# Kernel optimization log

Hardware: AMD Instinct MI355X
Metric: run time of the kernel (lower is better)

Reference implementation:

```python
import jax, jax.numpy as jnp
import numpy as np

TEMPERATURE = 0.1


def setup_inputs() -> dict:
    key = jax.random.key(0)
    k1, k2 = jax.random.split(key)
    B, D = 4096, 256
    z_i = jax.random.normal(k1, (B, D), dtype=jnp.float32)
    z_j = jax.random.normal(k2, (B, D), dtype=jnp.float32)
    return {"z_i": z_i, "z_j": z_j}


def reference(z_i, z_j):
    B = z_i.shape[0]
    N = 2 * B
    z = jnp.concatenate([z_i, z_j], axis=0)  # [N, D]
    # cosine similarity via normalize + GEMM (same math as broadcasted F.cosine_similarity)
    eps = 1e-8
    zn = z / jnp.maximum(jnp.linalg.norm(z, axis=1, keepdims=True), eps)
    sim = (zn @ zn.T) / TEMPERATURE  # [N, N]
    # positives: sim[i, (i+B) % N]
    rows = jnp.arange(N)
    pos = sim[rows, (rows + B) % N]  # [N]
    # denominator: sum of exp over all entries except the diagonal (positives included,
    # matching the original which only masks the eye)
    neg_inf = jnp.array(-jnp.inf, sim.dtype)
    sim_masked = jnp.where(jnp.eye(N, dtype=bool), neg_inf, sim)
    lse = jax.nn.logsumexp(sim_masked, axis=1)  # [N]
    loss = -(pos - lse)
    return loss.mean()
```

## Files before the change

### kernel.cpp

```cpp
#include <hip/hip_runtime.h>
#include <hip/hip_bf16.h>

typedef __bf16 bf16x8 __attribute__((ext_vector_type(8)));
typedef float  f32x4  __attribute__((ext_vector_type(4)));

#define N_TOT  8192
#define B_HALF 4096
#define D      256
#define SQK1   3.79828254f
#define LN2    0.6931471805599453f

#define RB      128
#define WROWS   32
#define CB      32
#define SLICE   512
#define NSLICE  16
#define NSTAGE  16

__global__ __launch_bounds__(256) void normalize_kernel(
    const float* __restrict__ zi, const float* __restrict__ zj,
    ushort* __restrict__ zn, float* __restrict__ out)
{
    if (blockIdx.x == 0 && threadIdx.x == 0) *out = 0.0f;
    int row  = (blockIdx.x * 256 + threadIdx.x) >> 6;
    int lane = threadIdx.x & 63;
    const float* src = (row < B_HALF) ? (zi + (size_t)row * D)
                                      : (zj + (size_t)(row - B_HALF) * D);
    float4 v = ((const float4*)src)[lane];
    float ss = v.x * v.x + v.y * v.y + v.z * v.z + v.w * v.w;
    #pragma unroll
    for (int m = 1; m < 64; m <<= 1) ss += __shfl_xor(ss, m);
    float r = SQK1 / fmaxf(sqrtf(ss), 1e-8f);
    union { ushort4 u4; __hip_bfloat16 h[4]; } o;
    o.h[0] = __float2bfloat16(v.x * r);
    o.h[1] = __float2bfloat16(v.y * r);
    o.h[2] = __float2bfloat16(v.z * r);
    o.h[3] = __float2bfloat16(v.w * r);
    ((ushort4*)zn)[(size_t)row * (D / 4) + lane] = o.u4;
}

__global__ __launch_bounds__(256) void fused_kernel(
    const ushort* __restrict__ zn,
    float* __restrict__ spartial,
    float* __restrict__ posdot)
{
    __shared__ ushort lds[2][CB * 256];

    int tid  = threadIdx.x;
    int lane = tid & 63;
    int w    = tid >> 6;
    int l15  = lane & 15;
    int l4   = lane >> 4;
    int r0   = blockIdx.x * RB + w * WROWS;
    int cs0  = blockIdx.y * SLICE;

    bf16x8 a[2][8];
    #pragma unroll
    for (int rt = 0; rt < 2; ++rt) {
        const ushort* ar = zn + (size_t)(r0 + rt * 16 + l15) * D + l4 * 8;
        #pragma unroll
        for (int kc = 0; kc < 8; ++kc)
            a[rt][kc] = *(const bf16x8*)(ar + kc * 32);
    }

    float srow[2][4];
    #pragma unroll
    for (int rt = 0; rt < 2; ++rt)
        #pragma unroll
        for (int g = 0; g < 4; ++g) srow[rt][g] = 0.f;

    uint4 st[4];
    #pragma unroll
    for (int i = 0; i < 4; ++i) {
        int chunk = tid + i * 256;
        st[i] = *(const uint4*)(zn + (size_t)(cs0 + (chunk >> 5)) * D + (chunk & 31) * 8);
    }
    #pragma unroll
    for (int i = 0; i < 4; ++i) {
        int chunk = tid + i * 256;
        int col = chunk >> 5, k16 = chunk & 31;
        *(uint4*)(&lds[0][col * 256 + ((k16 * 8) ^ ((col & 7) << 3))]) = st[i];
    }
    __syncthreads();

    int swzr = (lane & 7) << 3;

    for (int s = 0; s < NSTAGE; ++s) {
        int cur = s & 1;
        if (s + 1 < NSTAGE) {
            #pragma unroll
            for (int i = 0; i < 4; ++i) {
                int chunk = tid + i * 256;
                st[i] = *(const uint4*)(zn + (size_t)(cs0 + (s + 1) * CB + (chunk >> 5)) * D + (chunk & 31) * 8);
            }
        }

        f32x4 acc[2][2] = {};
        __builtin_amdgcn_s_setprio(1);
        #pragma unroll
        for (int kc = 0; kc < 8; ++kc) {
            #pragma unroll
            for (int ct = 0; ct < 2; ++ct) {
                int col = ct * 16 + l15;
                bf16x8 b = *(const bf16x8*)(&lds[cur][col * 256 + ((kc * 32 + l4 * 8) ^ swzr)]);
                acc[0][ct] = __builtin_amdgcn_mfma_f32_16x16x32_bf16(a[0][kc], b, acc[0][ct], 0, 0, 0);
                acc[1][ct] = __builtin_amdgcn_mfma_f32_16x16x32_bf16(a[1][kc], b, acc[1][ct], 0, 0, 0);
            }
        }
        __builtin_amdgcn_s_setprio(0);

        #pragma unroll
        for (int rt = 0; rt < 2; ++rt) {
            int rowb = r0 + rt * 16;
            #pragma unroll
            for (int ct = 0; ct < 2; ++ct) {
                int colb = cs0 + s * CB + ct * 16;
                bool isdiag = (rowb == colb);
                bool ispos  = ((rowb ^ B_HALF) == colb);
                if (isdiag) {
                    #pragma unroll
                    for (int g = 0; g < 4; ++g) {
                        int rl = l4 * 4 + g;
                        float e = exp2f(acc[rt][ct][g]);
                        srow[rt][g] += (rl != l15) ? e : 0.0f;
                    }
                } else if (ispos) {
                    #pragma unroll
                    for (int g = 0; g < 4; ++g) {
                        int rl = l4 * 4 + g;
                        if (rl == l15) posdot[rowb + rl] = acc[rt][ct][g];
                        srow[rt][g] += exp2f(acc[rt][ct][g]);
                    }
                } else {
                    #pragma unroll
                    for (int g = 0; g < 4; ++g)
                        srow[rt][g] += exp2f(acc[rt][ct][g]);
                }
            }
        }

        if (s + 1 < NSTAGE) {
            __syncthreads();
            #pragma unroll
            for (int i = 0; i < 4; ++i) {
                int chunk = tid + i * 256;
                int col = chunk >> 5, k16 = chunk & 31;
                *(uint4*)(&lds[cur ^ 1][col * 256 + ((k16 * 8) ^ ((col & 7) << 3))]) = st[i];
            }
            __syncthreads();
        }
    }

    #pragma unroll
    for (int rt = 0; rt < 2; ++rt) {
        #pragma unroll
        for (int g = 0; g < 4; ++g) {
            float v = srow[rt][g];
            v += __shfl_xor(v, 1);
            v += __shfl_xor(v, 2);
            v += __shfl_xor(v, 4);
            v += __shfl_xor(v, 8);
            if (l15 == 0) {
                int row = r0 + rt * 16 + l4 * 4 + g;
                spartial[(size_t)row * NSLICE + blockIdx.y] = v;
            }
        }
    }
}

__global__ __launch_bounds__(256) void finalize_kernel(
    const float* __restrict__ spartial, const float* __restrict__ posdot,
    float* __restrict__ out)
{
    int i    = blockIdx.x * 256 + threadIdx.x;
    int lane = threadIdx.x & 63;
    int wv   = threadIdx.x >> 6;
    float ssum = 0.f;
    #pragma unroll
    for (int k = 0; k < NSLICE; ++k) ssum += spartial[(size_t)i * NSLICE + k];
    float loss = LN2 * (log2f(ssum) - posdot[i]);
    #pragma unroll
    for (int m = 1; m < 64; m <<= 1) loss += __shfl_xor(loss, m);
    __shared__ float red[4];
    if (lane == 0) red[wv] = loss;
    __syncthreads();
    if (threadIdx.x == 0) {
        float t = red[0] + red[1] + red[2] + red[3];
        atomicAdd(out, t * (1.0f / (float)N_TOT));
    }
}

extern "C" void kernel_launch(void* const* d_in, const int* in_sizes, int n_in,
                              void* d_out, int out_size, void* d_ws, size_t ws_size,
                              hipStream_t stream)
{
    const float* zi = (const float*)d_in[0];
    const float* zj = (const float*)d_in[1];
    float* out = (float*)d_out;

    ushort* zn       = (ushort*)d_ws;
    float*  posdot   = (float*)((char*)d_ws + (size_t)N_TOT * D * 2);
    float*  spartial = (float*)((char*)d_ws + (size_t)N_TOT * D * 2 + N_TOT * 4);

    normalize_kernel<<<N_TOT / 4, 256, 0, stream>>>(zi, zj, zn, out);

    dim3 grid2(N_TOT / RB, NSLICE);
    fused_kernel<<<grid2, 256, 0, stream>>>(zn, spartial, posdot);

    finalize_kernel<<<N_TOT / 256, 256, 0, stream>>>(spartial, posdot, out);
}
```

Measured before the change: 142.9 us.

## Pad LDS rows, use raw v_exp_f32, transpose partial-sum layout, drop setprio

Replaces the XOR-swizzled LDS layout with padded rows (264 elements) and simplifies address computation by hoisting global and LDS pointers out of the loop. Uses the raw v_exp_f32 instruction through inline asm in place of exp2f, skipping range-handling code. Stores the per-slice partial sums slice-major so finalize reads are coalesced. Also removes the s_setprio calls around the MFMA loop. Padding may change bank-conflict behaviour, and the raw exp drops denormal handling.

```diff
diff --git a/kernel.cpp b/kernel.cpp
--- a/kernel.cpp
+++ b/kernel.cpp
@@ -11,11 +11,17 @@
 #define LN2    0.6931471805599453f
 
 #define RB      128
-#define WROWS   32
 #define CB      32
 #define SLICE   512
 #define NSLICE  16
 #define NSTAGE  16
+#define LDS_RS  264
+
+__device__ __forceinline__ float hexp2(float x) {
+    float r;
+    asm("v_exp_f32 %0, %1" : "=v"(r) : "v"(x));
+    return r;
+}
 
 __global__ __launch_bounds__(256) void normalize_kernel(
     const float* __restrict__ zi, const float* __restrict__ zj,
@@ -44,14 +50,14 @@
     float* __restrict__ spartial,
     float* __restrict__ posdot)
 {
-    __shared__ ushort lds[2][CB * 256];
+    __shared__ ushort lds[2][CB * LDS_RS];
 
     int tid  = threadIdx.x;
     int lane = tid & 63;
     int w    = tid >> 6;
     int l15  = lane & 15;
     int l4   = lane >> 4;
-    int r0   = blockIdx.x * RB + w * WROWS;
+    int r0   = blockIdx.x * RB + w * 32;
     int cs0  = blockIdx.y * SLICE;
 
     bf16x8 a[2][8];
@@ -69,45 +75,38 @@
         #pragma unroll
         for (int g = 0; g < 4; ++g) srow[rt][g] = 0.f;
 
+    const int col0 = tid >> 5, k16 = tid & 31;
+    const ushort* gsrc = zn + (size_t)(cs0 + col0) * D + k16 * 8;
+    const int lwr = col0 * LDS_RS + k16 * 8;
+
     uint4 st[4];
     #pragma unroll
-    for (int i = 0; i < 4; ++i) {
-        int chunk = tid + i * 256;
-        st[i] = *(const uint4*)(zn + (size_t)(cs0 + (chunk >> 5)) * D + (chunk & 31) * 8);
-    }
-    #pragma unroll
-    for (int i = 0; i < 4; ++i) {
-        int chunk = tid + i * 256;
-        int col = chunk >> 5, k16 = chunk & 31;
-        *(uint4*)(&lds[0][col * 256 + ((k16 * 8) ^ ((col & 7) << 3))]) = st[i];
-    }
+    for (int i = 0; i < 4; ++i) st[i] = *(const uint4*)(gsrc + i * 8 * D);
+    gsrc += (size_t)CB * D;
+    #pragma unroll
+    for (int i = 0; i < 4; ++i) *(uint4*)(&lds[0][lwr + i * 8 * LDS_RS]) = st[i];
     __syncthreads();
 
-    int swzr = (lane & 7) << 3;
+    const int lrd = l15 * LDS_RS + l4 * 8;
 
     for (int s = 0; s < NSTAGE; ++s) {
         int cur = s & 1;
         if (s + 1 < NSTAGE) {
             #pragma unroll
-            for (int i = 0; i < 4; ++i) {
-                int chunk = tid + i * 256;
-                st[i] = *(const uint4*)(zn + (size_t)(cs0 + (s + 1) * CB + (chunk >> 5)) * D + (chunk & 31) * 8);
-            }
+            for (int i = 0; i < 4; ++i) st[i] = *(const uint4*)(gsrc + i * 8 * D);
+            gsrc += (size_t)CB * D;
         }
 
         f32x4 acc[2][2] = {};
-        __builtin_amdgcn_s_setprio(1);
         #pragma unroll
         for (int kc = 0; kc < 8; ++kc) {
             #pragma unroll
             for (int ct = 0; ct < 2; ++ct) {
-                int col = ct * 16 + l15;
-                bf16x8 b = *(const bf16x8*)(&lds[cur][col * 256 + ((kc * 32 + l4 * 8) ^ swzr)]);
+                bf16x8 b = *(const bf16x8*)(&lds[cur][lrd + ct * 16 * LDS_RS + kc * 32]);
                 acc[0][ct] = __builtin_amdgcn_mfma_f32_16x16x32_bf16(a[0][kc], b, acc[0][ct], 0, 0, 0);
                 acc[1][ct] = __builtin_amdgcn_mfma_f32_16x16x32_bf16(a[1][kc], b, acc[1][ct], 0, 0, 0);
             }
         }
-        __builtin_amdgcn_s_setprio(0);
 
         #pragma unroll
         for (int rt = 0; rt < 2; ++rt) {
@@ -121,7 +120,7 @@
                     #pragma unroll
                     for (int g = 0; g < 4; ++g) {
                         int rl = l4 * 4 + g;
-                        float e = exp2f(acc[rt][ct][g]);
+                        float e = hexp2(acc[rt][ct][g]);
                         srow[rt][g] += (rl != l15) ? e : 0.0f;
                     }
                 } else if (ispos) {
@@ -129,12 +128,12 @@
                     for (int g = 0; g < 4; ++g) {
                         int rl = l4 * 4 + g;
                         if (rl == l15) posdot[rowb + rl] = acc[rt][ct][g];
-                        srow[rt][g] += exp2f(acc[rt][ct][g]);
+                        srow[rt][g] += hexp2(acc[rt][ct][g]);
                     }
                 } else {
                     #pragma unroll
                     for (int g = 0; g < 4; ++g)
-                        srow[rt][g] += exp2f(acc[rt][ct][g]);
+                        srow[rt][g] += hexp2(acc[rt][ct][g]);
                 }
             }
         }
@@ -142,11 +141,7 @@
         if (s + 1 < NSTAGE) {
             __syncthreads();
             #pragma unroll
-            for (int i = 0; i < 4; ++i) {
-                int chunk = tid + i * 256;
-                int col = chunk >> 5, k16 = chunk & 31;
-                *(uint4*)(&lds[cur ^ 1][col * 256 + ((k16 * 8) ^ ((col & 7) << 3))]) = st[i];
-            }
+            for (int i = 0; i < 4; ++i) *(uint4*)(&lds[cur ^ 1][lwr + i * 8 * LDS_RS]) = st[i];
             __syncthreads();
         }
     }
@@ -162,7 +157,7 @@
             v += __shfl_xor(v, 8);
             if (l15 == 0) {
                 int row = r0 + rt * 16 + l4 * 4 + g;
-                spartial[(size_t)row * NSLICE + blockIdx.y] = v;
+                spartial[(size_t)blockIdx.y * N_TOT + row] = v;
             }
         }
     }
@@ -177,7 +172,7 @@
     int wv   = threadIdx.x >> 6;
     float ssum = 0.f;
     #pragma unroll
-    for (int k = 0; k < NSLICE; ++k) ssum += spartial[(size_t)i * NSLICE + k];
+    for (int k = 0; k < NSLICE; ++k) ssum += spartial[(size_t)k * N_TOT + i];
     float loss = LN2 * (log2f(ssum) - posdot[i]);
     #pragma unroll
     for (int m = 1; m < 64; m <<= 1) loss += __shfl_xor(loss, m);
```

After: 163.4 us. +14.4%, slower.
